# Optimization experiments

Hardware: AMD Instinct MI355X
Metric: run time of the kernel (lower is better)

Reference implementation:

```python
import jax, jax.numpy as jnp
import numpy as np

IN_DIM = 256
OUT_DIM = 256
GRID_SIZE = 8
K = 3  # spline_order
LOW, UP = -1.0, 1.0
BATCH = 512


def _control_grid():
    # equally spaced control points, extended by K on each side (paper sec 2.4)
    spacing = (UP - LOW) / GRID_SIZE
    g = jnp.arange(-K, GRID_SIZE + K + 1, dtype=jnp.float32) * spacing + LOW
    # buffer shape (out_dim, in_dim, G + 2K + 1)
    return jnp.broadcast_to(g[None, None, :], (OUT_DIM, IN_DIM, g.shape[0]))


def _bspline_bases(x, grid):
    # x: (B, in_dim); grid: (out, in, T). Cox-de Boor recursion.
    xx = x[:, None, :, None]          # (B, 1, in, 1)
    g = grid[None]                    # (1, out, in, T)
    # order-0 (piecewise-constant) bases
    b = ((xx >= g[..., :-1]) & (xx < g[..., 1:])).astype(x.dtype)
    for j in range(1, K + 1):
        b = (xx - g[..., :-(j + 1)]) / (g[..., j:-1] - g[..., :-(j + 1)]) * b[..., :-1] \
          + (g[..., j + 1:] - xx) / (g[..., j + 1:] - g[..., 1:-j]) * b[..., 1:]
    return b  # (B, out, in, G + K)


def setup_inputs() -> dict:
    key = jax.random.key(0)
    k1, k2, k3 = jax.random.split(key, 3)
    x = jax.random.normal(k1, (BATCH, IN_DIM), dtype=jnp.float32)
    # xavier_normal_ on (out, in, G+K): fan_in = in*(G+K) -> std = sqrt(2/(fan_in+fan_out))
    fan_out = IN_DIM * (GRID_SIZE + K)  # torch convention: dim0 = fan_out, rest = fan_in
    fan_in = OUT_DIM * (GRID_SIZE + K)
    std = float(np.sqrt(2.0 / (fan_in + fan_out)))
    coef = jax.random.normal(k2, (OUT_DIM, IN_DIM, GRID_SIZE + K), dtype=jnp.float32) * std
    residual_weight = jax.random.normal(k3, (OUT_DIM, IN_DIM), dtype=jnp.float32) * 0.1
    univariate_weight = jnp.ones((OUT_DIM, IN_DIM), dtype=jnp.float32)
    return {"x": x, "coef": coef, "residual_weight": residual_weight,
            "univariate_weight": univariate_weight}


def reference(x, coef, residual_weight, univariate_weight):
    grid = _control_grid()
    bases = _bspline_bases(x, grid)                      # (B, out, in, G+K)
    spline = jnp.einsum('boig,oig->boi', bases, coef)    # sum over grid dim
    phi = residual_weight[None, :, :] * jax.nn.silu(x)[:, None, :] \
        + univariate_weight[None, :, :] * spline          # (B, out, in)
    return jnp.sum(phi, axis=-1)                          # (B, out)
```

## Files before the change

### kernel.cpp

```cpp
#include <hip/hip_runtime.h>
#include <hip/hip_bf16.h>

typedef unsigned short ushort_t;
typedef unsigned int uint_t;
typedef __attribute__((ext_vector_type(8))) short short8;
typedef __attribute__((ext_vector_type(4))) float f32x4;

#define IN_DIM 256
#define OUT_DIM 256
#define BATCH 512
#define NSPL 11
#define KSLOT 12
#define KDIM (IN_DIM * KSLOT)
#define BKU 384
#define NCHUNK 8

__device__ __forceinline__ uint_t pk2(float lo, float hi) {
  __hip_bfloat162 h = __float22bfloat162_rn(make_float2(lo, hi));
  union { __hip_bfloat162 h2; uint_t u; } c; c.h2 = h;
  return c.u;
}

__global__ __launch_bounds__(256) void build_aw(const float* __restrict__ x,
                                                const float* __restrict__ coef,
                                                const float* __restrict__ rw,
                                                const float* __restrict__ uw,
                                                ushort_t* __restrict__ A,
                                                ushort_t* __restrict__ W) {
  __shared__ float rowc[IN_DIM * NSPL];
  __shared__ __attribute__((aligned(8))) ushort_t stage[IN_DIM * KSLOT + 8];
  const int bx = blockIdx.x;
  const int t = threadIdx.x;

  if (bx < BATCH) {
    const float xf = x[bx * IN_DIM + t];
    const float tt = (xf + 1.75f) * 4.0f;
    const float fJ = floorf(tt);
    const int J = (int)fJ;
    const float u = tt - fJ;
    const float u2 = u * u, u3 = u2 * u, um = 1.0f - u;
    const float n0 = um * um * um * (1.0f / 6.0f);
    const float n1 = 0.5f * u3 - u2 + (4.0f / 6.0f);
    const float n2 = -0.5f * u3 + 0.5f * u2 + 0.5f * u + (1.0f / 6.0f);
    const float n3 = u3 * (1.0f / 6.0f);
    const float silu = xf / (1.0f + __expf(-xf));

    ushort_t* cb = &stage[t * KSLOT];
    ushort_t* dump = &stage[IN_DIM * KSLOT];
    *(unsigned long long*)&cb[0] = 0ull;
    *(unsigned long long*)&cb[4] = 0ull;
    *(unsigned long long*)&cb[8] = 0ull;

    const uint_t p01 = pk2(n0, n1);
    const uint_t p23 = pk2(n2, n3);
    const uint_t psl = pk2(silu, silu);
    const int base = J - 3;
    ushort_t* w0 = ((unsigned)(base + 0) <= 10u) ? (cb + base + 0) : (dump + 0);
    ushort_t* w1 = ((unsigned)(base + 1) <= 10u) ? (cb + base + 1) : (dump + 1);
    ushort_t* w2 = ((unsigned)(base + 2) <= 10u) ? (cb + base + 2) : (dump + 2);
    ushort_t* w3 = ((unsigned)(base + 3) <= 10u) ? (cb + base + 3) : (dump + 3);
    *w0 = (ushort_t)p01;
    *w1 = (ushort_t)(p01 >> 16);
    *w2 = (ushort_t)p23;
    *w3 = (ushort_t)(p23 >> 16);
    cb[11] = (ushort_t)psl;
    __syncthreads();

    uint_t* dst = (uint_t*)(A + (size_t)bx * KDIM);
    const uint_t* src = (const uint_t*)stage;
#pragma unroll
    for (int p = 0; p < 6; ++p) dst[t + p * 256] = src[t + p * 256];
  } else {
    const int o = bx - BATCH;
    const float* src = coef + (size_t)o * IN_DIM * NSPL;
#pragma unroll
    for (int j = 0; j < 11; ++j) rowc[t + j * 256] = src[t + j * 256];
    __syncthreads();

    const float us = uw[o * IN_DIM + t];
    const float r  = rw[o * IN_DIM + t];
    const float* c = &rowc[t * NSPL];
    uint_t* cell = (uint_t*)&stage[t * KSLOT];
    cell[0] = pk2(us * c[0], us * c[1]);
    cell[1] = pk2(us * c[2], us * c[3]);
    cell[2] = pk2(us * c[4], us * c[5]);
    cell[3] = pk2(us * c[6], us * c[7]);
    cell[4] = pk2(us * c[8], us * c[9]);
    cell[5] = pk2(us * c[10], r);
    __syncthreads();

    uint_t* dst = (uint_t*)(W + (size_t)o * KDIM);
    const uint_t* s2 = (const uint_t*)stage;
#pragma unroll
    for (int p = 0; p < 6; ++p) dst[t + p * 256] = s2[t + p * 256];
  }
}

__global__ __launch_bounds__(256, 3) void gemm(const ushort_t* __restrict__ A,
                                               const ushort_t* __restrict__ W,
                                               float* __restrict__ out) {
  __shared__ __attribute__((aligned(16))) ushort_t As[2][16 * BKU];
  __shared__ __attribute__((aligned(16))) ushort_t Ws[2][16 * BKU];
  __shared__ f32x4 red[3][64];

  const int tid = threadIdx.x;
  const int lane = tid & 63;
  const int w = tid >> 6;
  const int B = blockIdx.x;
  const int mt = B >> 4;
  const int nt = ((B & 7) << 1) | ((B >> 3) & 1);
  const int b0 = mt * 16, o0 = nt * 16;
  const int mn = lane & 15;
  const int klane = (lane >> 4) * 8;

  int srcOff[3], ldsOff[3];
#pragma unroll
  for (int i = 0; i < 3; ++i) {
    const int F = ((w * 3 + i) * 64 + lane) * 8;
    const int rowi = F / BKU;
    const int coli = F % BKU;
    srcOff[i] = rowi * KDIM + coli;
    ldsOff[i] = rowi * BKU + (coli ^ ((rowi & 7) << 3));
  }
  const ushort_t* Ap = A + (size_t)b0 * KDIM;
  const ushort_t* Wp = W + (size_t)o0 * KDIM;

  const int mrow = mn * BKU;
  const int msw = (mn & 7) << 3;

  f32x4 acc = {0.f, 0.f, 0.f, 0.f};

  short8 s0a0, s0a1, s0a2, s0w0, s0w1, s0w2;
  short8 s1a0, s1a1, s1a2, s1w0, s1w1, s1w2;

#define ISSUE_S0(C) { const int kb = (C) * BKU;                               \
    s0a0 = *(const short8*)(Ap + srcOff[0] + kb);                             \
    s0a1 = *(const short8*)(Ap + srcOff[1] + kb);                             \
    s0a2 = *(const short8*)(Ap + srcOff[2] + kb);                             \
    s0w0 = *(const short8*)(Wp + srcOff[0] + kb);                             \
    s0w1 = *(const short8*)(Wp + srcOff[1] + kb);                             \
    s0w2 = *(const short8*)(Wp + srcOff[2] + kb); }
#define ISSUE_S1(C) { const int kb = (C) * BKU;                               \
    s1a0 = *(const short8*)(Ap + srcOff[0] + kb);                             \
    s1a1 = *(const short8*)(Ap + srcOff[1] + kb);                             \
    s1a2 = *(const short8*)(Ap + srcOff[2] + kb);                             \
    s1w0 = *(const short8*)(Wp + srcOff[0] + kb);                             \
    s1w1 = *(const short8*)(Wp + srcOff[1] + kb);                             \
    s1w2 = *(const short8*)(Wp + srcOff[2] + kb); }
#define COMMIT_S0(BUF) {                                                      \
    *(short8*)&As[BUF][ldsOff[0]] = s0a0;                                     \
    *(short8*)&As[BUF][ldsOff[1]] = s0a1;                                     \
    *(short8*)&As[BUF][ldsOff[2]] = s0a2;                                     \
    *(short8*)&Ws[BUF][ldsOff[0]] = s0w0;                                     \
    *(short8*)&Ws[BUF][ldsOff[1]] = s0w1;                                     \
    *(short8*)&Ws[BUF][ldsOff[2]] = s0w2; }
#define COMMIT_S1(BUF) {                                                      \
    *(short8*)&As[BUF][ldsOff[0]] = s1a0;                                     \
    *(short8*)&As[BUF][ldsOff[1]] = s1a1;                                     \
    *(short8*)&As[BUF][ldsOff[2]] = s1a2;                                     \
    *(short8*)&Ws[BUF][ldsOff[0]] = s1w0;                                     \
    *(short8*)&Ws[BUF][ldsOff[1]] = s1w1;                                     \
    *(short8*)&Ws[BUF][ldsOff[2]] = s1w2; }

#define MFMA3(BUF) { _Pragma("unroll")                                        \
    for (int q = 0; q < 3; ++q) {                                             \
      const int kidx = w * 96 + q * 32 + klane;                               \
      const int idx = mrow + (kidx ^ msw);                                    \
      short8 af  = *(const short8*)&As[BUF][idx];                             \
      short8 bfr = *(const short8*)&Ws[BUF][idx];                             \
      acc = __builtin_amdgcn_mfma_f32_16x16x32_bf16(af, bfr, acc, 0, 0, 0); }}

  ISSUE_S0(0)
  COMMIT_S0(0)
  ISSUE_S1(1)
  __syncthreads();

#pragma unroll
  for (int cc = 0; cc < 4; ++cc) {
    if (cc < 3) { ISSUE_S0(2 * cc + 2) }
    MFMA3(0)
    COMMIT_S1(1)
    __syncthreads();

    if (cc < 3) {
      ISSUE_S1(2 * cc + 3)
      MFMA3(1)
      COMMIT_S0(0)
      __syncthreads();
    } else {
      MFMA3(1)
    }
  }

  if (w > 0) red[w - 1][lane] = acc;
  __syncthreads();

  if (w == 0) {
    const f32x4 t0 = red[0][lane];
    const f32x4 t1 = red[1][lane];
    const f32x4 t2 = red[2][lane];
#pragma unroll
    for (int q = 0; q < 4; ++q) acc[q] += t0[q] + t1[q] + t2[q];

    const int col = o0 + mn;
    const int rbase = b0 + (lane >> 4) * 4;
#pragma unroll
    for (int r = 0; r < 4; ++r) {
      out[(size_t)(rbase + r) * OUT_DIM + col] = acc[r];
    }
  }
}

extern "C" void kernel_launch(void* const* d_in, const int* in_sizes, int n_in,
                              void* d_out, int out_size, void* d_ws, size_t ws_size,
                              hipStream_t stream) {
  const float* x    = (const float*)d_in[0];
  const float* coef = (const float*)d_in[1];
  const float* rw   = (const float*)d_in[2];
  const float* uw   = (const float*)d_in[3];
  float* out = (float*)d_out;

  ushort_t* A = (ushort_t*)d_ws;
  ushort_t* W = A + (size_t)BATCH * KDIM;

  build_aw<<<BATCH + OUT_DIM, 256, 0, stream>>>(x, coef, rw, uw, A, W);
  gemm<<<512, 256, 0, stream>>>(A, W, out);
}
```

Measured before the change: 17.43 us.

## Specialize GEMM warps into producer loaders and consumer MFMA warps

Splits the four waves of each GEMM block by role: waves 2 and 3 each load one operand (A or W) from global memory into LDS, and waves 0 and 1 run six MFMAs per stage over half of the K chunk. The cross-wave reduction drops from four partial sums to two. The aim is to overlap global loads with matrix math across waves instead of within each wave. The cost is that only half the waves do MFMA work, and loader waves hold 24 short8 registers, which may pressure occupancy.

```diff
diff --git a/kernel.cpp b/kernel.cpp
--- a/kernel.cpp
+++ b/kernel.cpp
@@ -13,7 +13,6 @@
 #define KSLOT 12
 #define KDIM (IN_DIM * KSLOT)
 #define BKU 384
-#define NCHUNK 8
 
 __device__ __forceinline__ uint_t pk2(float lo, float hi) {
   __hip_bfloat162 h = __float22bfloat162_rn(make_float2(lo, hi));
@@ -101,7 +100,7 @@
                                                float* __restrict__ out) {
   __shared__ __attribute__((aligned(16))) ushort_t As[2][16 * BKU];
   __shared__ __attribute__((aligned(16))) ushort_t Ws[2][16 * BKU];
-  __shared__ f32x4 red[3][64];
+  __shared__ f32x4 red[64];
 
   const int tid = threadIdx.x;
   const int lane = tid & 63;
@@ -113,94 +112,116 @@
   const int mn = lane & 15;
   const int klane = (lane >> 4) * 8;
 
-  int srcOff[3], ldsOff[3];
-#pragma unroll
-  for (int i = 0; i < 3; ++i) {
-    const int F = ((w * 3 + i) * 64 + lane) * 8;
-    const int rowi = F / BKU;
-    const int coli = F % BKU;
-    srcOff[i] = rowi * KDIM + coli;
-    ldsOff[i] = rowi * BKU + (coli ^ ((rowi & 7) << 3));
-  }
-  const ushort_t* Ap = A + (size_t)b0 * KDIM;
-  const ushort_t* Wp = W + (size_t)o0 * KDIM;
-
   const int mrow = mn * BKU;
   const int msw = (mn & 7) << 3;
 
+  int srcOff[12], ldsOff[12];
+  const ushort_t* SP = nullptr;
+  ushort_t* L0 = nullptr;
+  ushort_t* L1 = nullptr;
+  if (w >= 2) {
+#pragma unroll
+    for (int i = 0; i < 12; ++i) {
+      const int F = (i * 64 + lane) * 8;
+      const int rowi = F / BKU;
+      const int coli = F % BKU;
+      srcOff[i] = rowi * KDIM + coli;
+      ldsOff[i] = rowi * BKU + (coli ^ ((rowi & 7) << 3));
+    }
+    SP = (w == 2) ? (A + (size_t)b0 * KDIM) : (W + (size_t)o0 * KDIM);
+    L0 = (w == 2) ? &As[0][0] : &Ws[0][0];
+    L1 = (w == 2) ? &As[1][0] : &Ws[1][0];
+  }
+
   f32x4 acc = {0.f, 0.f, 0.f, 0.f};
 
-  short8 s0a0, s0a1, s0a2, s0w0, s0w1, s0w2;
-  short8 s1a0, s1a1, s1a2, s1w0, s1w1, s1w2;
-
-#define ISSUE_S0(C) { const int kb = (C) * BKU;                               \
-    s0a0 = *(const short8*)(Ap + srcOff[0] + kb);                             \
-    s0a1 = *(const short8*)(Ap + srcOff[1] + kb);                             \
-    s0a2 = *(const short8*)(Ap + srcOff[2] + kb);                             \
-    s0w0 = *(const short8*)(Wp + srcOff[0] + kb);                             \
-    s0w1 = *(const short8*)(Wp + srcOff[1] + kb);                             \
-    s0w2 = *(const short8*)(Wp + srcOff[2] + kb); }
-#define ISSUE_S1(C) { const int kb = (C) * BKU;                               \
-    s1a0 = *(const short8*)(Ap + srcOff[0] + kb);                             \
-    s1a1 = *(const short8*)(Ap + srcOff[1] + kb);                             \
-    s1a2 = *(const short8*)(Ap + srcOff[2] + kb);                             \
-    s1w0 = *(const short8*)(Wp + srcOff[0] + kb);                             \
-    s1w1 = *(const short8*)(Wp + srcOff[1] + kb);                             \
-    s1w2 = *(const short8*)(Wp + srcOff[2] + kb); }
-#define COMMIT_S0(BUF) {                                                      \
-    *(short8*)&As[BUF][ldsOff[0]] = s0a0;                                     \
-    *(short8*)&As[BUF][ldsOff[1]] = s0a1;                                     \
-    *(short8*)&As[BUF][ldsOff[2]] = s0a2;                                     \
-    *(short8*)&Ws[BUF][ldsOff[0]] = s0w0;                                     \
-    *(short8*)&Ws[BUF][ldsOff[1]] = s0w1;                                     \
-    *(short8*)&Ws[BUF][ldsOff[2]] = s0w2; }
-#define COMMIT_S1(BUF) {                                                      \
-    *(short8*)&As[BUF][ldsOff[0]] = s1a0;                                     \
-    *(short8*)&As[BUF][ldsOff[1]] = s1a1;                                     \
-    *(short8*)&As[BUF][ldsOff[2]] = s1a2;                                     \
-    *(short8*)&Ws[BUF][ldsOff[0]] = s1w0;                                     \
-    *(short8*)&Ws[BUF][ldsOff[1]] = s1w1;                                     \
-    *(short8*)&Ws[BUF][ldsOff[2]] = s1w2; }
-
-#define MFMA3(BUF) { _Pragma("unroll")                                        \
-    for (int q = 0; q < 3; ++q) {                                             \
-      const int kidx = w * 96 + q * 32 + klane;                               \
+  short8 g0, g1, g2, g3, g4, g5, g6, g7, g8, g9, g10, g11;
+  short8 h0, h1, h2, h3, h4, h5, h6, h7, h8, h9, h10, h11;
+
+#define ISSUE_G(C) { const int kb = (C) * BKU;                                \
+    g0  = *(const short8*)(SP + srcOff[0]  + kb);                             \
+    g1  = *(const short8*)(SP + srcOff[1]  + kb);                             \
+    g2  = *(const short8*)(SP + srcOff[2]  + kb);                             \
+    g3  = *(const short8*)(SP + srcOff[3]  + kb);                             \
+    g4  = *(const short8*)(SP + srcOff[4]  + kb);                             \
+    g5  = *(const short8*)(SP + srcOff[5]  + kb);                             \
+    g6  = *(const short8*)(SP + srcOff[6]  + kb);                             \
+    g7  = *(const short8*)(SP + srcOff[7]  + kb);                             \
+    g8  = *(const short8*)(SP + srcOff[8]  + kb);                             \
+    g9  = *(const short8*)(SP + srcOff[9]  + kb);                             \
+    g10 = *(const short8*)(SP + srcOff[10] + kb);                             \
+    g11 = *(const short8*)(SP + srcOff[11] + kb); }
+#define ISSUE_H(C) { const int kb = (C) * BKU;                                \
+    h0  = *(const short8*)(SP + srcOff[0]  + kb);                             \
+    h1  = *(const short8*)(SP + srcOff[1]  + kb);                             \
+    h2  = *(const short8*)(SP + srcOff[2]  + kb);                             \
+    h3  = *(const short8*)(SP + srcOff[3]  + kb);                             \
+    h4  = *(const short8*)(SP + srcOff[4]  + kb);                             \
+    h5  = *(const short8*)(SP + srcOff[5]  + kb);                             \
+    h6  = *(const short8*)(SP + srcOff[6]  + kb);                             \
+    h7  = *(const short8*)(SP + srcOff[7]  + kb);                             \
+    h8  = *(const short8*)(SP + srcOff[8]  + kb);                             \
+    h9  = *(const short8*)(SP + srcOff[9]  + kb);                             \
+    h10 = *(const short8*)(SP + srcOff[10] + kb);                             \
+    h11 = *(const short8*)(SP + srcOff[11] + kb); }
+#define COMMIT_G(LP) {                                                        \
+    *(short8*)&LP[ldsOff[0]]  = g0;  *(short8*)&LP[ldsOff[1]]  = g1;          \
+    *(short8*)&LP[ldsOff[2]]  = g2;  *(short8*)&LP[ldsOff[3]]  = g3;          \
+    *(short8*)&LP[ldsOff[4]]  = g4;  *(short8*)&LP[ldsOff[5]]  = g5;          \
+    *(short8*)&LP[ldsOff[6]]  = g6;  *(short8*)&LP[ldsOff[7]]  = g7;          \
+    *(short8*)&LP[ldsOff[8]]  = g8;  *(short8*)&LP[ldsOff[9]]  = g9;          \
+    *(short8*)&LP[ldsOff[10]] = g10; *(short8*)&LP[ldsOff[11]] = g11; }
+#define COMMIT_H(LP) {                                                        \
+    *(short8*)&LP[ldsOff[0]]  = h0;  *(short8*)&LP[ldsOff[1]]  = h1;          \
+    *(short8*)&LP[ldsOff[2]]  = h2;  *(short8*)&LP[ldsOff[3]]  = h3;          \
+    *(short8*)&LP[ldsOff[4]]  = h4;  *(short8*)&LP[ldsOff[5]]  = h5;          \
+    *(short8*)&LP[ldsOff[6]]  = h6;  *(short8*)&LP[ldsOff[7]]  = h7;          \
+    *(short8*)&LP[ldsOff[8]]  = h8;  *(short8*)&LP[ldsOff[9]]  = h9;          \
+    *(short8*)&LP[ldsOff[10]] = h10; *(short8*)&LP[ldsOff[11]] = h11; }
+
+#define MFMA6(BUF) { _Pragma("unroll")                                        \
+    for (int q = 0; q < 6; ++q) {                                             \
+      const int kidx = w * 192 + q * 32 + klane;                              \
       const int idx = mrow + (kidx ^ msw);                                    \
       short8 af  = *(const short8*)&As[BUF][idx];                             \
       short8 bfr = *(const short8*)&Ws[BUF][idx];                             \
       acc = __builtin_amdgcn_mfma_f32_16x16x32_bf16(af, bfr, acc, 0, 0, 0); }}
 
-  ISSUE_S0(0)
-  COMMIT_S0(0)
-  ISSUE_S1(1)
+  if (w >= 2) {
+    ISSUE_G(0)
+    COMMIT_G(L0)
+    ISSUE_H(1)
+  }
   __syncthreads();
 
 #pragma unroll
   for (int cc = 0; cc < 4; ++cc) {
-    if (cc < 3) { ISSUE_S0(2 * cc + 2) }
-    MFMA3(0)
-    COMMIT_S1(1)
-    __syncthreads();
-
-    if (cc < 3) {
-      ISSUE_S1(2 * cc + 3)
-      MFMA3(1)
-      COMMIT_S0(0)
-      __syncthreads();
+    if (w >= 2) {
+      if (cc < 3) { ISSUE_G(2 * cc + 2) }
+      COMMIT_H(L1)
     } else {
-      MFMA3(1)
-    }
-  }
-
-  if (w > 0) red[w - 1][lane] = acc;
+      MFMA6(0)
+    }
+    __syncthreads();
+
+    if (w >= 2) {
+      if (cc < 3) {
+        ISSUE_H(2 * cc + 3)
+        COMMIT_G(L0)
+      }
+    } else {
+      MFMA6(1)
+    }
+    if (cc < 3) __syncthreads();
+  }
+
+  if (w == 1) red[lane] = acc;
   __syncthreads();
 
   if (w == 0) {
-    const f32x4 t0 = red[0][lane];
-    const f32x4 t1 = red[1][lane];
-    const f32x4 t2 = red[2][lane];
-#pragma unroll
-    for (int q = 0; q < 4; ++q) acc[q] += t0[q] + t1[q] + t2[q];
+    const f32x4 t1 = red[lane];
+#pragma unroll
+    for (int q = 0; q < 4; ++q) acc[q] += t1[q];
 
     const int col = o0 + mn;
     const int rbase = b0 + (lane >> 4) * 4;
```

New measurement: 18.36 us. +5.3%, slower.
